# Kernel optimization log

Hardware: AMD Instinct MI355X
Metric: run time of the kernel (lower is better)

## Reference

```python
import jax, jax.numpy as jnp
import numpy as np

EPS = 1e-8
LRELU_ALPHA = 0.2
LRELU_GAIN = float(np.sqrt(2.0))


def setup_inputs() -> dict:
    key = jax.random.key(0)
    k1, k2, k3, k4 = jax.random.split(key, 4)
    N, Cin, Cout, T, H, W, K = 2, 128, 128, 16, 64, 64, 3
    x = jax.random.normal(k1, (N, Cin, T, H, W), dtype=jnp.float32)
    weight = jax.random.normal(k2, (Cout, Cin, K, K, K), dtype=jnp.float32)
    style = jax.random.normal(k3, (N, Cin, T), dtype=jnp.float32)
    bias = jax.random.normal(k4, (Cout,), dtype=jnp.float32)
    return {"x": x, "weight": weight, "style": style, "bias": bias}


def reference(x, weight, style, bias):
    # --- demodulate pre-normalization (max-abs) ---
    w = weight / jnp.max(jnp.abs(weight), axis=(1, 2, 3, 4), keepdims=True)
    s = style / jnp.max(jnp.abs(style), axis=(1, 2), keepdims=True)
    # fan-in gain
    fan_in = w.shape[1] * w.shape[2] * w.shape[3] * w.shape[4]
    w = w / np.sqrt(fan_in)
    # demodulation: [N, Cout, T]
    demod = jax.lax.rsqrt(jnp.einsum('oizyx,nit->not', w * w, s * s) + EPS)
    # per-timestep style modulation of the input
    xm = x * s[:, :, :, None, None]  # [N,Cin,T,H,W]
    # dense conv3d, 'same' padding for 3x3x3
    out = jax.lax.conv_general_dilated(
        xm, w.astype(xm.dtype),
        window_strides=(1, 1, 1),
        padding=[(1, 1), (1, 1), (1, 1)],
        dimension_numbers=('NCDHW', 'OIDHW', 'NCDHW'))
    out = out * demod[:, :, :, None, None].astype(out.dtype)
    # bias_act(lrelu) with StyleGAN gain sqrt(2)
    z = out + bias[None, :, None, None, None]
    return jnp.where(z >= 0, z, LRELU_ALPHA * z) * LRELU_GAIN
```

## Files before the change

### kernel.cpp

```cpp
#include <hip/hip_runtime.h>
#include <hip/hip_bf16.h>
#include <math.h>

typedef __attribute__((ext_vector_type(8))) short bf16x8;
typedef __attribute__((ext_vector_type(4))) float f32x4;

#define N_B  2
#define CIN  128
#define COUT 128
#define T_   16
#define H_   64
#define W_   64
#define FANIN 3456

#define OFF_WMAX   0
#define OFF_SMAX   512
#define OFF_SNORM  1024
#define OFF_WSQ    20480
#define OFF_DEMOD  86016
#define OFF_APACK  102400
#define OFF_ZERO   1048576
#define OFF_XMT    2097152
#define ZOFF       (-524288)

__global__ __launch_bounds__(256) void k_zero(uint4* __restrict__ zp) {
    #pragma unroll
    for (int k = 0; k < 4; ++k)
        zp[threadIdx.x + k * 256] = make_uint4(0u, 0u, 0u, 0u);
}

__global__ __launch_bounds__(256) void k_wmax(const float* __restrict__ w,
                                              float* __restrict__ wmax) {
    int o = blockIdx.x;
    const float* p = w + (size_t)o * FANIN;
    float m = 0.f;
    for (int i = threadIdx.x; i < FANIN; i += 256) m = fmaxf(m, fabsf(p[i]));
    __shared__ float red[256];
    red[threadIdx.x] = m; __syncthreads();
    for (int s = 128; s > 0; s >>= 1) {
        if (threadIdx.x < s) red[threadIdx.x] = fmaxf(red[threadIdx.x], red[threadIdx.x + s]);
        __syncthreads();
    }
    if (threadIdx.x == 0) wmax[o] = red[0];
}

__global__ __launch_bounds__(256) void k_smax(const float* __restrict__ s,
                                              float* __restrict__ smax) {
    int n = blockIdx.x;
    const float* p = s + (size_t)n * CIN * T_;
    float m = 0.f;
    for (int i = threadIdx.x; i < CIN * T_; i += 256) m = fmaxf(m, fabsf(p[i]));
    __shared__ float red[256];
    red[threadIdx.x] = m; __syncthreads();
    for (int q = 128; q > 0; q >>= 1) {
        if (threadIdx.x < q) red[threadIdx.x] = fmaxf(red[threadIdx.x], red[threadIdx.x + q]);
        __syncthreads();
    }
    if (threadIdx.x == 0) smax[n] = red[0];
}

__global__ __launch_bounds__(256) void k_snorm(const float* __restrict__ style,
                                               const float* __restrict__ smax,
                                               float* __restrict__ snorm) {
    int idx = blockIdx.x * 256 + threadIdx.x;
    if (idx < N_B * CIN * T_) {
        int n = idx / (CIN * T_);
        snorm[idx] = style[idx] / smax[n];
    }
}

__global__ __launch_bounds__(128) void k_wpack(const float* __restrict__ w,
                                               const float* __restrict__ wmax,
                                               ushort* __restrict__ apack,
                                               float* __restrict__ wsq) {
    int o = blockIdx.x, i = threadIdx.x;
    float inv = 1.0f / (wmax[o] * sqrtf((float)FANIN));
    const float* p = w + ((size_t)o * CIN + i) * 27;
    int c = i >> 5, ii = i & 31;
    int lane = (o & 15) + ((ii >> 3) << 4);
    int j = ii & 7;
    int m = o >> 4;
    size_t base = (((size_t)c * 8 + m) * 64 + lane) * 8 + j;
    float sq = 0.f;
    #pragma unroll
    for (int tap = 0; tap < 27; tap++) {
        float wn = p[tap] * inv;
        sq = fmaf(wn, wn, sq);
        __hip_bfloat16 hb = __float2bfloat16(wn);
        apack[base + (size_t)tap * 16384] = *(ushort*)&hb;
    }
    wsq[o * CIN + i] = sq;
}

__global__ __launch_bounds__(128) void k_demod(const float* __restrict__ wsq,
                                               const float* __restrict__ snorm,
                                               float* __restrict__ demod) {
    int nt = blockIdx.x;
    int n = nt / T_, t = nt % T_;
    __shared__ float s2[CIN];
    int tid = threadIdx.x;
    float sv = snorm[(n * CIN + tid) * T_ + t];
    s2[tid] = sv * sv;
    __syncthreads();
    const float* wq = wsq + tid * CIN;
    float d = 0.f;
    for (int i = 0; i < CIN; i++) d = fmaf(wq[i], s2[i], d);
    demod[(n * COUT + tid) * T_ + t] = 1.0f / sqrtf(d + 1e-8f);
}

__global__ __launch_bounds__(256) void k_xmt(const float* __restrict__ x,
                                             const float* __restrict__ snorm,
                                             ushort* __restrict__ xmt) {
    __shared__ float lds[CIN * 65];
    int bid = blockIdx.x;
    int h = bid & 63, t = (bid >> 6) & 15, n = bid >> 10;
    int tid = threadIdx.x;
    int wl = tid & 63, cq = tid >> 6;
    for (int pass = 0; pass < 32; pass++) {
        int ci = pass * 4 + cq;
        float s = snorm[(n * CIN + ci) * T_ + t];
        float v = x[(((size_t)(n * CIN + ci) * T_ + t) * H_ + h) * W_ + wl] * s;
        lds[ci * 65 + wl] = v;
    }
    __syncthreads();
    int ci2 = tid & 63, wq = tid >> 6;
    uint* dst = (uint*)xmt;
    for (int pass = 0; pass < 16; pass++) {
        int w = pass * 4 + wq;
        float f0 = lds[(2 * ci2) * 65 + w];
        float f1 = lds[(2 * ci2 + 1) * 65 + w];
        __hip_bfloat16 h0 = __float2bfloat16(f0);
        __hip_bfloat16 h1 = __float2bfloat16(f1);
        uint pk = (uint)(*(ushort*)&h0) | ((uint)(*(ushort*)&h1) << 16);
        dst[((((size_t)(n * T_ + t) * H_ + h) * W_ + w)) * 64 + ci2] = pk;
    }
}

__global__ __launch_bounds__(512, 2) void k_conv(const ushort* __restrict__ xmt,
                                                 const ushort* __restrict__ apack,
                                                 const float* __restrict__ demod,
                                                 const float* __restrict__ bias,
                                                 float* __restrict__ out) {
    __shared__ ushort __attribute__((aligned(16))) xs[65536];

    int bid = blockIdx.x;
    int h8 = bid & 7, t = (bid >> 3) & 15, n = bid >> 7;
    int hbase = h8 * 8;
    int tid = threadIdx.x;
    int lane = tid & 63;
    int wid = tid >> 6;
    int mrow = wid & 1;
    int hp = wid >> 1;
    int lw = lane & 15, lg = lane >> 4;

    int goff[16];
    #pragma unroll
    for (int k = 0; k < 16; ++k) {
        int idx = tid + (k << 9);
        int off = ZOFF;
        if (idx < 7920) {
            int w = idx % 66;
            int r = idx / 66;
            int g = r & 3;
            int q = r >> 2;
            int tz = q / 10, hh = q % 10;
            int gt = t + tz - 1, gh = hbase + hh - 1, gw = w - 1;
            if ((unsigned)gt < T_ && (unsigned)gh < H_ && (unsigned)gw < W_)
                off = (((n * 16 + gt) * 64 + gh) * 64 + gw) * 128 + g * 8;
        }
        goff[k] = off;
    }

#define STAGE(cc) do { \
    _Pragma("unroll") \
    for (int k = 0; k < 16; ++k) \
        __builtin_amdgcn_global_load_lds( \
            (const __attribute__((address_space(1))) void*)(xmt + goff[k] + (cc) * 32), \
            (__attribute__((address_space(3))) void*)((char*)xs + ((size_t)tid + (k << 9)) * 16), \
            16, 0, 0); \
} while (0)

    f32x4 acc[4][8];
    #pragma unroll
    for (int i = 0; i < 4; i++)
        #pragma unroll
        for (int jn = 0; jn < 8; jn++)
            acc[i][jn] = (f32x4){0.f, 0.f, 0.f, 0.f};

    bf16x8 A0[4], A1[4];

#define LOADA(BANK, TAP) do { \
    const ushort* ap_ = apc + (TAP) * 16384; \
    BANK[0] = *(const bf16x8*)(ap_); \
    BANK[1] = *(const bf16x8*)(ap_ + 512); \
    BANK[2] = *(const bf16x8*)(ap_ + 1024); \
    BANK[3] = *(const bf16x8*)(ap_ + 1536); \
} while (0)

#define TAPC(BANK, TAP) do { \
    const int tz_ = (TAP) / 9, dy_ = ((TAP) / 3) % 3, dx_ = (TAP) % 3; \
    const int q0_ = tz_ * 10 + dy_; \
    const ushort* br0_ = &xs[(((q0_ + hp * 2 + 0) * 4 + lg) * 66 + lw) * 8 + dx_ * 8]; \
    const ushort* br1_ = &xs[(((q0_ + hp * 2 + 1) * 4 + lg) * 66 + lw) * 8 + dx_ * 8]; \
    bf16x8 b00_ = *(const bf16x8*)(br0_); \
    bf16x8 b01_ = *(const bf16x8*)(br0_ + 128); \
    bf16x8 b02_ = *(const bf16x8*)(br0_ + 256); \
    bf16x8 b03_ = *(const bf16x8*)(br0_ + 384); \
    bf16x8 b10_ = *(const bf16x8*)(br1_); \
    bf16x8 b11_ = *(const bf16x8*)(br1_ + 128); \
    bf16x8 b12_ = *(const bf16x8*)(br1_ + 256); \
    bf16x8 b13_ = *(const bf16x8*)(br1_ + 384); \
    _Pragma("unroll") \
    for (int mi_ = 0; mi_ < 4; ++mi_) { \
        acc[mi_][0] = __builtin_amdgcn_mfma_f32_16x16x32_bf16(BANK[mi_], b00_, acc[mi_][0], 0, 0, 0); \
        acc[mi_][1] = __builtin_amdgcn_mfma_f32_16x16x32_bf16(BANK[mi_], b01_, acc[mi_][1], 0, 0, 0); \
        acc[mi_][2] = __builtin_amdgcn_mfma_f32_16x16x32_bf16(BANK[mi_], b02_, acc[mi_][2], 0, 0, 0); \
        acc[mi_][3] = __builtin_amdgcn_mfma_f32_16x16x32_bf16(BANK[mi_], b03_, acc[mi_][3], 0, 0, 0); \
        acc[mi_][4] = __builtin_amdgcn_mfma_f32_16x16x32_bf16(BANK[mi_], b10_, acc[mi_][4], 0, 0, 0); \
        acc[mi_][5] = __builtin_amdgcn_mfma_f32_16x16x32_bf16(BANK[mi_], b11_, acc[mi_][5], 0, 0, 0); \
        acc[mi_][6] = __builtin_amdgcn_mfma_f32_16x16x32_bf16(BANK[mi_], b12_, acc[mi_][6], 0, 0, 0); \
        acc[mi_][7] = __builtin_amdgcn_mfma_f32_16x16x32_bf16(BANK[mi_], b13_, acc[mi_][7], 0, 0, 0); \
    } \
} while (0)

#define UNIT(ULD, UCMP, TNEXT, TCUR) \
    LOADA(ULD, TNEXT); __builtin_amdgcn_sched_barrier(0); TAPC(UCMP, TCUR);

    for (int c = 0; c < 4; ++c) {
        if (c) __syncthreads();
        STAGE(c);
        __syncthreads();

        const ushort* apc = apack + (c * 4096 + mrow * 2048 + lane * 8);

        LOADA(A0, 0);
        UNIT(A1, A0,  1,  0)  UNIT(A0, A1,  2,  1)  UNIT(A1, A0,  3,  2)
        UNIT(A0, A1,  4,  3)  UNIT(A1, A0,  5,  4)  UNIT(A0, A1,  6,  5)
        UNIT(A1, A0,  7,  6)  UNIT(A0, A1,  8,  7)  UNIT(A1, A0,  9,  8)
        UNIT(A0, A1, 10,  9)  UNIT(A1, A0, 11, 10)  UNIT(A0, A1, 12, 11)
        UNIT(A1, A0, 13, 12)  UNIT(A0, A1, 14, 13)  UNIT(A1, A0, 15, 14)
        UNIT(A0, A1, 16, 15)  UNIT(A1, A0, 17, 16)  UNIT(A0, A1, 18, 17)
        UNIT(A1, A0, 19, 18)  UNIT(A0, A1, 20, 19)  UNIT(A1, A0, 21, 20)
        UNIT(A0, A1, 22, 21)  UNIT(A1, A0, 23, 22)  UNIT(A0, A1, 24, 23)
        UNIT(A1, A0, 25, 24)  UNIT(A0, A1, 26, 25)
        TAPC(A0, 26);
    }
#undef UNIT
#undef LOADA
#undef TAPC
#undef STAGE

    #pragma unroll
    for (int mi = 0; mi < 4; mi++) {
        #pragma unroll
        for (int r = 0; r < 4; r++) {
            int o = mrow * 64 + mi * 16 + lg * 4 + r;
            float d = demod[(n * COUT + o) * T_ + t];
            float bv = bias[o];
            #pragma unroll
            for (int rl = 0; rl < 2; rl++) {
                int h = hbase + hp * 2 + rl;
                #pragma unroll
                for (int ws = 0; ws < 4; ws++) {
                    float z = fmaf(acc[mi][rl * 4 + ws][r], d, bv);
                    z = (z >= 0.f ? z : 0.2f * z) * 1.41421356237309515f;
                    out[(((size_t)(n * COUT + o) * T_ + t) * H_ + h) * W_ + ws * 16 + lw] = z;
                }
            }
        }
    }
}

extern "C" void kernel_launch(void* const* d_in, const int* in_sizes, int n_in,
                              void* d_out, int out_size, void* d_ws, size_t ws_size,
                              hipStream_t stream) {
    const float* x      = (const float*)d_in[0];
    const float* weight = (const float*)d_in[1];
    const float* style  = (const float*)d_in[2];
    const float* bias   = (const float*)d_in[3];
    float* out = (float*)d_out;

    char* ws = (char*)d_ws;
    float*  wmax  = (float*)(ws + OFF_WMAX);
    float*  smax  = (float*)(ws + OFF_SMAX);
    float*  snorm = (float*)(ws + OFF_SNORM);
    float*  wsq   = (float*)(ws + OFF_WSQ);
    float*  demod = (float*)(ws + OFF_DEMOD);
    uint4*  zpage = (uint4*)(ws + OFF_ZERO);
    ushort* apack = (ushort*)(ws + OFF_APACK);
    ushort* xmt   = (ushort*)(ws + OFF_XMT);

    k_zero <<<1, 256, 0, stream>>>(zpage);
    k_wmax <<<COUT, 256, 0, stream>>>(weight, wmax);
    k_smax <<<N_B, 256, 0, stream>>>(style, smax);
    k_snorm<<<(N_B * CIN * T_ + 255) / 256, 256, 0, stream>>>(style, smax, snorm);
    k_wpack<<<COUT, 128, 0, stream>>>(weight, wmax, apack, wsq);
    k_demod<<<N_B * T_, 128, 0, stream>>>(wsq, snorm, demod);
    k_xmt  <<<N_B * T_ * H_, 256, 0, stream>>>(x, snorm, xmt);

    k_conv<<<N_B * T_ * (H_ / 8), 512, 0, stream>>>(xmt, apack, demod, bias, out);
}
```

Measured before the change: 147.1 us.

## Retile conv to 4-row blocks with each wave covering all 128 output channels

```diff
diff --git a/kernel.cpp b/kernel.cpp
--- a/kernel.cpp
+++ b/kernel.cpp
@@ -136,34 +136,32 @@
     }
 }
 
-__global__ __launch_bounds__(512, 2) void k_conv(const ushort* __restrict__ xmt,
+__global__ __launch_bounds__(256, 2) void k_conv(const ushort* __restrict__ xmt,
                                                  const ushort* __restrict__ apack,
                                                  const float* __restrict__ demod,
                                                  const float* __restrict__ bias,
                                                  float* __restrict__ out) {
-    __shared__ ushort __attribute__((aligned(16))) xs[65536];
+    __shared__ ushort __attribute__((aligned(16))) xs[38912];
 
     int bid = blockIdx.x;
-    int h8 = bid & 7, t = (bid >> 3) & 15, n = bid >> 7;
-    int hbase = h8 * 8;
+    int h4 = bid & 15, t = (bid >> 4) & 15, n = bid >> 8;
+    int hbase = h4 * 4;
     int tid = threadIdx.x;
     int lane = tid & 63;
-    int wid = tid >> 6;
-    int mrow = wid & 1;
-    int hp = wid >> 1;
+    int hq = tid >> 6;
     int lw = lane & 15, lg = lane >> 4;
 
-    int goff[16];
-    #pragma unroll
-    for (int k = 0; k < 16; ++k) {
-        int idx = tid + (k << 9);
+    int goff[19];
+    #pragma unroll
+    for (int k = 0; k < 19; ++k) {
+        int idx = tid + (k << 8);
         int off = ZOFF;
-        if (idx < 7920) {
+        if (idx < 4752) {
             int w = idx % 66;
             int r = idx / 66;
             int g = r & 3;
             int q = r >> 2;
-            int tz = q / 10, hh = q % 10;
+            int tz = q / 6, hh = q % 6;
             int gt = t + tz - 1, gh = hbase + hh - 1, gw = w - 1;
             if ((unsigned)gt < T_ && (unsigned)gh < H_ && (unsigned)gw < W_)
                 off = (((n * 16 + gt) * 64 + gh) * 64 + gw) * 128 + g * 8;
@@ -173,53 +171,43 @@
 
 #define STAGE(cc) do { \
     _Pragma("unroll") \
-    for (int k = 0; k < 16; ++k) \
+    for (int k = 0; k < 19; ++k) \
         __builtin_amdgcn_global_load_lds( \
             (const __attribute__((address_space(1))) void*)(xmt + goff[k] + (cc) * 32), \
-            (__attribute__((address_space(3))) void*)((char*)xs + ((size_t)tid + (k << 9)) * 16), \
+            (__attribute__((address_space(3))) void*)((char*)xs + ((size_t)tid + (k << 8)) * 16), \
             16, 0, 0); \
 } while (0)
 
-    f32x4 acc[4][8];
-    #pragma unroll
-    for (int i = 0; i < 4; i++)
+    f32x4 acc[8][4];
+    #pragma unroll
+    for (int i = 0; i < 8; i++)
         #pragma unroll
-        for (int jn = 0; jn < 8; jn++)
+        for (int jn = 0; jn < 4; jn++)
             acc[i][jn] = (f32x4){0.f, 0.f, 0.f, 0.f};
 
-    bf16x8 A0[4], A1[4];
+    bf16x8 A0[8], A1[8];
 
 #define LOADA(BANK, TAP) do { \
     const ushort* ap_ = apc + (TAP) * 16384; \
-    BANK[0] = *(const bf16x8*)(ap_); \
-    BANK[1] = *(const bf16x8*)(ap_ + 512); \
-    BANK[2] = *(const bf16x8*)(ap_ + 1024); \
-    BANK[3] = *(const bf16x8*)(ap_ + 1536); \
+    _Pragma("unroll") \
+    for (int f_ = 0; f_ < 8; ++f_) \
+        BANK[f_] = *(const bf16x8*)(ap_ + f_ * 512); \
 } while (0)
 
 #define TAPC(BANK, TAP) do { \
     const int tz_ = (TAP) / 9, dy_ = ((TAP) / 3) % 3, dx_ = (TAP) % 3; \
-    const int q0_ = tz_ * 10 + dy_; \
-    const ushort* br0_ = &xs[(((q0_ + hp * 2 + 0) * 4 + lg) * 66 + lw) * 8 + dx_ * 8]; \
-    const ushort* br1_ = &xs[(((q0_ + hp * 2 + 1) * 4 + lg) * 66 + lw) * 8 + dx_ * 8]; \
-    bf16x8 b00_ = *(const bf16x8*)(br0_); \
-    bf16x8 b01_ = *(const bf16x8*)(br0_ + 128); \
-    bf16x8 b02_ = *(const bf16x8*)(br0_ + 256); \
-    bf16x8 b03_ = *(const bf16x8*)(br0_ + 384); \
-    bf16x8 b10_ = *(const bf16x8*)(br1_); \
-    bf16x8 b11_ = *(const bf16x8*)(br1_ + 128); \
-    bf16x8 b12_ = *(const bf16x8*)(br1_ + 256); \
-    bf16x8 b13_ = *(const bf16x8*)(br1_ + 384); \
+    const int q_ = tz_ * 6 + hq + dy_; \
+    const ushort* bb_ = &xs[((q_ * 4 + lg) * 66 + lw) * 8 + dx_ * 8]; \
+    bf16x8 b0_ = *(const bf16x8*)(bb_); \
+    bf16x8 b1_ = *(const bf16x8*)(bb_ + 128); \
+    bf16x8 b2_ = *(const bf16x8*)(bb_ + 256); \
+    bf16x8 b3_ = *(const bf16x8*)(bb_ + 384); \
     _Pragma("unroll") \
-    for (int mi_ = 0; mi_ < 4; ++mi_) { \
-        acc[mi_][0] = __builtin_amdgcn_mfma_f32_16x16x32_bf16(BANK[mi_], b00_, acc[mi_][0], 0, 0, 0); \
-        acc[mi_][1] = __builtin_amdgcn_mfma_f32_16x16x32_bf16(BANK[mi_], b01_, acc[mi_][1], 0, 0, 0); \
-        acc[mi_][2] = __builtin_amdgcn_mfma_f32_16x16x32_bf16(BANK[mi_], b02_, acc[mi_][2], 0, 0, 0); \
-        acc[mi_][3] = __builtin_amdgcn_mfma_f32_16x16x32_bf16(BANK[mi_], b03_, acc[mi_][3], 0, 0, 0); \
-        acc[mi_][4] = __builtin_amdgcn_mfma_f32_16x16x32_bf16(BANK[mi_], b10_, acc[mi_][4], 0, 0, 0); \
-        acc[mi_][5] = __builtin_amdgcn_mfma_f32_16x16x32_bf16(BANK[mi_], b11_, acc[mi_][5], 0, 0, 0); \
-        acc[mi_][6] = __builtin_amdgcn_mfma_f32_16x16x32_bf16(BANK[mi_], b12_, acc[mi_][6], 0, 0, 0); \
-        acc[mi_][7] = __builtin_amdgcn_mfma_f32_16x16x32_bf16(BANK[mi_], b13_, acc[mi_][7], 0, 0, 0); \
+    for (int mi_ = 0; mi_ < 8; ++mi_) { \
+        acc[mi_][0] = __builtin_amdgcn_mfma_f32_16x16x32_bf16(BANK[mi_], b0_, acc[mi_][0], 0, 0, 0); \
+        acc[mi_][1] = __builtin_amdgcn_mfma_f32_16x16x32_bf16(BANK[mi_], b1_, acc[mi_][1], 0, 0, 0); \
+        acc[mi_][2] = __builtin_amdgcn_mfma_f32_16x16x32_bf16(BANK[mi_], b2_, acc[mi_][2], 0, 0, 0); \
+        acc[mi_][3] = __builtin_amdgcn_mfma_f32_16x16x32_bf16(BANK[mi_], b3_, acc[mi_][3], 0, 0, 0); \
     } \
 } while (0)
 
@@ -231,7 +219,7 @@
         STAGE(c);
         __syncthreads();
 
-        const ushort* apc = apack + (c * 4096 + mrow * 2048 + lane * 8);
+        const ushort* apc = apack + (c * 4096 + lane * 8);
 
         LOADA(A0, 0);
         UNIT(A1, A0,  1,  0)  UNIT(A0, A1,  2,  1)  UNIT(A1, A0,  3,  2)
@@ -250,22 +238,19 @@
 #undef TAPC
 #undef STAGE
 
-    #pragma unroll
-    for (int mi = 0; mi < 4; mi++) {
+    int h = hbase + hq;
+    #pragma unroll
+    for (int mi = 0; mi < 8; mi++) {
         #pragma unroll
         for (int r = 0; r < 4; r++) {
-            int o = mrow * 64 + mi * 16 + lg * 4 + r;
+            int o = mi * 16 + lg * 4 + r;
             float d = demod[(n * COUT + o) * T_ + t];
             float bv = bias[o];
             #pragma unroll
-            for (int rl = 0; rl < 2; rl++) {
-                int h = hbase + hp * 2 + rl;
-                #pragma unroll
-                for (int ws = 0; ws < 4; ws++) {
-                    float z = fmaf(acc[mi][rl * 4 + ws][r], d, bv);
-                    z = (z >= 0.f ? z : 0.2f * z) * 1.41421356237309515f;
-                    out[(((size_t)(n * COUT + o) * T_ + t) * H_ + h) * W_ + ws * 16 + lw] = z;
-                }
+            for (int nb = 0; nb < 4; nb++) {
+                float z = fmaf(acc[mi][nb][r], d, bv);
+                z = (z >= 0.f ? z : 0.2f * z) * 1.41421356237309515f;
+                out[(((size_t)(n * COUT + o) * T_ + t) * H_ + h) * W_ + nb * 16 + lw] = z;
             }
         }
     }
@@ -298,5 +283,5 @@
     k_demod<<<N_B * T_, 128, 0, stream>>>(wsq, snorm, demod);
     k_xmt  <<<N_B * T_ * H_, 256, 0, stream>>>(x, snorm, xmt);
 
-    k_conv<<<N_B * T_ * (H_ / 8), 512, 0, stream>>>(xmt, apack, demod, bias, out);
-}
+    k_conv<<<N_B * T_ * (H_ / 4), 256, 0, stream>>>(xmt, apack, demod, bias, out);
+}
```

Result: slower. 161.3 us (+9.6%).
